# Kernel optimization log

Hardware: AMD Instinct MI355X
Metric: run time of the kernel (lower is better)

Reference implementation:

```python
import jax, jax.numpy as jnp
import numpy as np

B, K, N, D, H, NNEG, NTOP = 8, 8, 128, 256, 128, 64, 64
UNARY_SCALES = (1.0, 1.0, 1.0)  # one scale per tree level, tree_height = log2(K) = 3


def setup_inputs():
    key = jax.random.key(0)
    ks = jax.random.split(key, 8)
    s = 0.05
    return {
        'pos_fea': jax.random.normal(ks[0], (B, K, N, D), jnp.float32),
        'neg_fea': jax.random.normal(ks[1], (B * K, NNEG, D), jnp.float32),
        'pos_classes': jax.random.randint(ks[2], (B, K, N), 0, 20),
        'target_class': jax.random.randint(ks[3], (B,), 0, 20),
        'Wp1': jax.random.normal(ks[4], (2 * D, H), jnp.float32) * s,
        'bp1': jnp.zeros((H,), jnp.float32),
        'Wp2': jax.random.normal(ks[5], (H, 1), jnp.float32) * s,
        'bp2': jnp.zeros((1,), jnp.float32),
        'Wu1': jax.random.normal(ks[6], (2 * D, H), jnp.float32) * s,
        'bu1': jnp.zeros((H,), jnp.float32),
        'Wu2': jax.random.normal(ks[7], (H, 1), jnp.float32) * s,
        'bu2': jnp.zeros((1,), jnp.float32),
    }


def _relation(f0, f1, W1, b1, W2, b2):
    # RelationModule: Dense(H, relu) -> Dense(1) applied to concat([f0_m, f1_n])
    # for every cross pair; concat-Dense is split into two GEMMs. -> [Bn, M0, M1]
    d = f0.shape[-1]
    h0 = jnp.einsum('bmd,dh->bmh', f0, W1[:d])
    h1 = jnp.einsum('bnd,dh->bnh', f1, W1[d:])
    h = jax.nn.relu(h0[:, :, None, :] + h1[:, None, :, :] + b1)
    return jnp.einsum('bmnh,h->bmn', h, W2[:, 0]) + b2[0]


def _bg(t, idx):
    # batched_gather along axis 1: t [Bn, P, ...], idx [Bn, T]
    ie = idx.reshape(idx.shape + (1,) * (t.ndim - 2))
    ie = jnp.broadcast_to(ie, idx.shape + t.shape[2:])
    return jnp.take_along_axis(t, ie, axis=1)


def _rep(fea, sub):
    # subproblem representative feature: fea [Bn,S,N,D], sub [Bn,M,S] -> [Bn,M,D]
    idx = jnp.swapaxes(sub, 1, 2)[..., None]              # [Bn,S,M,1]
    idx = jnp.broadcast_to(idx, idx.shape[:-1] + (fea.shape[-1],))
    return jnp.take_along_axis(fea, idx, axis=2).mean(axis=1)


def _tree(pos_fea, neg_fea, Wp1, bp1, Wp2, bp2, Wu1, bu1, Wu2, bu2):
    pos_flat = pos_fea.reshape(B * K, N, D)
    # UnaryModule: mean relation score of each positive proposal vs the negative bag
    ue = _relation(pos_flat, neg_fea, Wu1, bu1, Wu2, bu2).mean(-1)   # [B*K, N]
    sub = jnp.broadcast_to(jnp.arange(N, dtype=jnp.int32)[None, :, None], (B * K, N, 1))
    pe = jnp.zeros_like(ue)
    tree_height = int(np.log2(K))
    best = None
    for i in range(tree_height):
        S = 2 ** i                      # subproblem size per branch at this level
        Bn = sub.shape[0] // 2
        M = sub.shape[1]
        sub2 = sub.reshape(Bn, 2, M, S)  # [::2] / [1::2] split of adjacent rows
        sub0, sub1 = sub2[:, 0], sub2[:, 1]
        pe2 = pe.reshape(Bn, 2, M)
        ue2 = ue.reshape(Bn, 2, M)
        fea = pos_flat.reshape(Bn, 2, S, N, D)
        rep0 = _rep(fea[:, 0], sub0)
        rep1 = _rep(fea[:, 1], sub1)
        # PairwiseCrossSimilarity: scores for all cross pairs of candidates
        scores = _relation(rep0, rep1, Wp1, bp1, Wp2, bp2).reshape(Bn, M * M)
        p0 = jnp.repeat(jnp.arange(M), M)
        p1 = jnp.tile(jnp.arange(M), M)
        pe = pe2[:, 0][:, p0] + pe2[:, 1][:, p1] - scores
        ue = ue2[:, 0][:, p0] + ue2[:, 1][:, p1]
        total = pe + UNARY_SCALES[i] * ue
        sub = jnp.concatenate([sub0[:, p0], sub1[:, p1]], axis=-1)  # [Bn, M*M, 2S]
        topk = 1 if i == tree_height - 1 else min(M * M, NTOP)
        _, inds = jax.lax.top_k(-total, topk)
        sub = _bg(sub, inds)
        ue = jnp.take_along_axis(ue, inds, axis=1)
        pe = jnp.take_along_axis(pe, inds, axis=1)
        best = jnp.take_along_axis(total, inds, axis=1)
    return sub, best


def reference(pos_fea, neg_fea, pos_classes, target_class,
              Wp1, bp1, Wp2, bp2, Wu1, bu1, Wu2, bu2):
    sub, _ = _tree(pos_fea, neg_fea, Wp1, bp1, Wp2, bp2, Wu1, bu1, Wu2, bu2)
    is_target = (pos_classes == target_class[:, None, None]).astype(jnp.float32)
    return sub[:, 0], is_target  # selected proposal per image [B,K], [B,K,N]
```

## Files before the change

### kernel.cpp

```cpp
#include <hip/hip_runtime.h>
#include <stdint.h>

#define B_ 8
#define K_ 8
#define N_ 128
#define D_ 256
#define H_ 128
#define NNEG_ 64

typedef unsigned long long u64;

__device__ __forceinline__ u64 shfl_xor_u64(u64 v, int m) {
    int lo = __shfl_xor((int)(unsigned)v, m, 64);
    int hi = __shfl_xor((int)(unsigned)(v >> 32), m, 64);
    return ((u64)(unsigned)hi << 32) | (unsigned)lo;
}
__device__ __forceinline__ u64 bitonic_merge64(u64 m, int lane) {
#pragma unroll
    for (int j = 32; j > 0; j >>= 1) {
        u64 o = shfl_xor_u64(m, j);
        bool keepMin = ((lane & j) == 0);
        bool lt = m < o;
        m = (keepMin == lt) ? m : o;
    }
    return m;
}
__device__ __forceinline__ u64 merge2(u64 a, u64 b, int lane) {
    u64 br = shfl_xor_u64(b, 63);
    u64 m = a < br ? a : br;
    return bitonic_merge64(m, lane);
}
__device__ __forceinline__ unsigned sortable(float f) {
    unsigned u = __float_as_uint(f);
    return (u & 0x80000000u) ? ~u : (u | 0x80000000u);
}
__device__ __forceinline__ float unsortable(unsigned u) {
    return __uint_as_float((u & 0x80000000u) ? (u & 0x7FFFFFFFu) : ~u);
}
__device__ __forceinline__ void sort128_reg(u64& v0, u64& v1, int lane) {
#pragma unroll
    for (int k = 2; k <= 64; k <<= 1) {
        bool d0 = ((lane & k) == 0);
        bool d1 = (k == 64) ? false : d0;
#pragma unroll
        for (int j = k >> 1; j > 0; j >>= 1) {
            u64 o0 = shfl_xor_u64(v0, j);
            bool km0 = (((lane & j) == 0) == d0);
            v0 = (km0 == (v0 < o0)) ? v0 : o0;
            u64 o1 = shfl_xor_u64(v1, j);
            bool km1 = (((lane & j) == 0) == d1);
            v1 = (km1 == (v1 < o1)) ? v1 : o1;
        }
    }
    if (v0 > v1) { u64 tmp = v0; v0 = v1; v1 = tmp; }
#pragma unroll
    for (int j = 32; j > 0; j >>= 1) {
        bool km = ((lane & j) == 0);
        u64 o0 = shfl_xor_u64(v0, j);
        v0 = (km == (v0 < o0)) ? v0 : o0;
        u64 o1 = shfl_xor_u64(v1, j);
        v1 = (km == (v1 < o1)) ? v1 : o1;
    }
}

__global__ __launch_bounds__(256) void g1_gemm(
    const float* __restrict__ pos, const float* __restrict__ neg,
    const float* __restrict__ Wu1, const float* __restrict__ Wp1,
    const int* __restrict__ pos_classes, const int* __restrict__ target_class,
    float* __restrict__ HU0, float* __restrict__ HU1n,
    float* __restrict__ HP0, float* __restrict__ HP1,
    float* __restrict__ outp) {
    int bid = blockIdx.x;
    int t = threadIdx.x;
    if (bid >= 896) {
        int base = (bid - 896) * 2048 + t * 8;
#pragma unroll
        for (int q = 0; q < 8; ++q) {
            int idx = base + q;
            outp[64 + idx] = (pos_classes[idx] == target_class[idx >> 10]) ? 1.0f : 0.0f;
        }
        return;
    }
    const float* A; const float* W; float* OUT; int bid2;
    if (bid < 256)      { A = pos; W = Wu1;           OUT = HU0;  bid2 = bid; }
    else if (bid < 384) { A = neg; W = Wu1 + D_ * H_; OUT = HU1n; bid2 = bid - 256; }
    else if (bid < 640) { A = pos; W = Wp1;           OUT = HP0;  bid2 = bid - 384; }
    else                { A = pos; W = Wp1 + D_ * H_; OUT = HP1;  bid2 = bid - 640; }
    int rb = (bid2 >> 1) * 64;
    int cb64 = (bid2 & 1) * 64;

    __shared__ float AsT[32][68];
    __shared__ float Bs[32][64];
    int tx = t & 15, ty = t >> 4;
    float acc[4][4];
#pragma unroll
    for (int i = 0; i < 4; ++i)
#pragma unroll
        for (int j = 0; j < 4; ++j) acc[i][j] = 0.f;

    for (int k0 = 0; k0 < D_; k0 += 32) {
#pragma unroll
        for (int rep = 0; rep < 2; ++rep) {
            int flat = t + rep * 256;
            int row = flat >> 3, kq = flat & 7;
            const float4 av = *(const float4*)&A[(size_t)(rb + row) * D_ + k0 + kq * 4];
            AsT[kq * 4 + 0][row] = av.x;
            AsT[kq * 4 + 1][row] = av.y;
            AsT[kq * 4 + 2][row] = av.z;
            AsT[kq * 4 + 3][row] = av.w;
        }
#pragma unroll
        for (int rep = 0; rep < 2; ++rep) {
            int flat = t + rep * 256;
            int kr = flat >> 4, cq = flat & 15;
            *(float4*)&Bs[kr][cq * 4] =
                *(const float4*)&W[(size_t)(k0 + kr) * H_ + cb64 + cq * 4];
        }
        __syncthreads();
#pragma unroll 8
        for (int kk = 0; kk < 32; ++kk) {
            const float4 av = *(const float4*)&AsT[kk][ty * 4];
            const float4 bv = *(const float4*)&Bs[kk][tx * 4];
            acc[0][0] += av.x * bv.x; acc[0][1] += av.x * bv.y;
            acc[0][2] += av.x * bv.z; acc[0][3] += av.x * bv.w;
            acc[1][0] += av.y * bv.x; acc[1][1] += av.y * bv.y;
            acc[1][2] += av.y * bv.z; acc[1][3] += av.y * bv.w;
            acc[2][0] += av.z * bv.x; acc[2][1] += av.z * bv.y;
            acc[2][2] += av.z * bv.z; acc[2][3] += av.z * bv.w;
            acc[3][0] += av.w * bv.x; acc[3][1] += av.w * bv.y;
            acc[3][2] += av.w * bv.z; acc[3][3] += av.w * bv.w;
        }
        __syncthreads();
    }
#pragma unroll
    for (int i = 0; i < 4; ++i) {
        float4 o = {acc[i][0], acc[i][1], acc[i][2], acc[i][3]};
        *(float4*)&OUT[(size_t)(rb + ty * 4 + i) * H_ + cb64 + tx * 4] = o;
    }
}

__global__ __launch_bounds__(256) void g2_ue_sc0(
    const float* __restrict__ HU0, const float* __restrict__ HU1n,
    const float* __restrict__ bu1, const float* __restrict__ Wu2,
    const float* __restrict__ bu2v,
    const float* __restrict__ HP0, const float* __restrict__ HP1,
    const float* __restrict__ bp1, const float* __restrict__ Wp2,
    const float* __restrict__ bp2,
    float* __restrict__ t0, float* __restrict__ sc0) {
    __shared__ float LsT[128][36];
    __shared__ float RsT[128][66];
    __shared__ float wsv[128];
    __shared__ float red[32][33];

    int bid = blockIdx.x;
    int t = threadIdx.x;
    bool is_ue = bid < 256;

    const float* Lsrc; const float* Rsrc; const float* b1v; const float* W2;
    if (is_ue) {
        int bk = bid >> 2, mt = bid & 3;
        Lsrc = HU0 + (size_t)(bk * N_ + mt * 32) * H_;
        Rsrc = HU1n + (size_t)bk * NNEG_ * H_;
        b1v = bu1; W2 = Wu2;
    } else {
        int bid2 = bid - 256;
        int b = bid2 >> 3, m0t = (bid2 >> 1) & 3, m1t = bid2 & 1;
        Lsrc = HP0 + (size_t)b * 2 * N_ * H_ + m0t * 32 * H_;
        Rsrc = HP1 + (size_t)b * 2 * N_ * H_ + N_ * H_ + m1t * 64 * H_;
        b1v = bp1; W2 = Wp2;
    }
    for (int i = t; i < 32 * 32; i += 256) {
        int m = i & 31, hq = i >> 5;
        const float4 a = *(const float4*)&Lsrc[(size_t)m * H_ + hq * 4];
        const float4 b = *(const float4*)&b1v[hq * 4];
        LsT[hq * 4 + 0][m] = a.x + b.x;
        LsT[hq * 4 + 1][m] = a.y + b.y;
        LsT[hq * 4 + 2][m] = a.z + b.z;
        LsT[hq * 4 + 3][m] = a.w + b.w;
    }
    for (int i = t; i < 64 * 32; i += 256) {
        int n = i & 63, hq = i >> 6;
        const float4 a = *(const float4*)&Rsrc[(size_t)n * H_ + hq * 4];
        RsT[hq * 4 + 0][n] = a.x;
        RsT[hq * 4 + 1][n] = a.y;
        RsT[hq * 4 + 2][n] = a.z;
        RsT[hq * 4 + 3][n] = a.w;
    }
    if (t < 128) wsv[t] = W2[t];
    __syncthreads();

    int tm = t & 7, tn = t >> 3;
    float a00 = 0.f, a01 = 0.f, a10 = 0.f, a11 = 0.f;
    float a20 = 0.f, a21 = 0.f, a30 = 0.f, a31 = 0.f;
#pragma unroll 4
    for (int h = 0; h < 128; ++h) {
        const float4 lv = *(const float4*)&LsT[h][tm * 4];
        const float2 rv = *(const float2*)&RsT[h][tn * 2];
        float w = wsv[h];
        float v;
        v = lv.x + rv.x; v = v > 0.f ? v : 0.f; a00 += v * w;
        v = lv.x + rv.y; v = v > 0.f ? v : 0.f; a01 += v * w;
        v = lv.y + rv.x; v = v > 0.f ? v : 0.f; a10 += v * w;
        v = lv.y + rv.y; v = v > 0.f ? v : 0.f; a11 += v * w;
        v = lv.z + rv.x; v = v > 0.f ? v : 0.f; a20 += v * w;
        v = lv.z + rv.y; v = v > 0.f ? v : 0.f; a21 += v * w;
        v = lv.w + rv.x; v = v > 0.f ? v : 0.f; a30 += v * w;
        v = lv.w + rv.y; v = v > 0.f ? v : 0.f; a31 += v * w;
    }

    if (is_ue) {
        int bk = bid >> 2, mt = bid & 3;
        red[tm * 4 + 0][tn] = a00 + a01;
        red[tm * 4 + 1][tn] = a10 + a11;
        red[tm * 4 + 2][tn] = a20 + a21;
        red[tm * 4 + 3][tn] = a30 + a31;
        __syncthreads();
        if (t < 32) {
            float s = 0.f;
            for (int q = 0; q < 32; ++q) s += red[t][q];
            t0[bk * N_ + mt * 32 + t] = s * (1.0f / NNEG_) + bu2v[0];
        }
    } else {
        int bid2 = bid - 256;
        int b = bid2 >> 3, m0t = (bid2 >> 1) & 3, m1t = bid2 & 1;
        float bp2v = bp2[0];
        float* orow = sc0 + (size_t)b * 16384;
        float accs[4][2] = {{a00, a01}, {a10, a11}, {a20, a21}, {a30, a31}};
#pragma unroll
        for (int i = 0; i < 4; ++i) {
            int m0 = m0t * 32 + tm * 4 + i;
#pragma unroll
            for (int j = 0; j < 2; ++j) {
                int m1 = m1t * 64 + tn * 2 + j;
                orow[m0 * 128 + m1] = accs[i][j] + bp2v;
            }
        }
    }
}

__global__ __launch_bounds__(256) void g3a_top0(const float* __restrict__ sc0,
                                                const float* __restrict__ t0,
                                                u64* __restrict__ g3c) {
    int bid = blockIdx.x;
    int r = bid >> 3, c = bid & 7;
    int t = threadIdx.x, lane = t & 63, w = t >> 6;
    __shared__ float tt[256];
    __shared__ u64 cand[4][128];
    if (t < 256) tt[t] = t0[r * 256 + t];
    __syncthreads();
    const float* row = sc0 + (size_t)r * 16384 + c * 2048 + w * 512;
    unsigned sv[8];
#pragma unroll
    for (int j = 0; j < 8; ++j) {
        int li = j * 64 + lane;
        int idx = c * 2048 + w * 512 + li;
        float v = (tt[idx >> 7] + tt[128 + (idx & 127)]) - row[li];
        sv[j] = sortable(v);
    }
    unsigned T = 0u;
#pragma unroll
    for (int it = 0; it < 16; ++it) {
        int p = 30 - 2 * it;
        unsigned C1 = T | (1u << p), C2 = T | (2u << p), C3 = T | (3u << p);
        unsigned c1 = 0u, c2 = 0u, c3 = 0u;
#pragma unroll
        for (int j = 0; j < 8; ++j) {
            c1 += (unsigned)__popcll(__ballot(sv[j] < C1));
            c2 += (unsigned)__popcll(__ballot(sv[j] < C2));
            c3 += (unsigned)__popcll(__ballot(sv[j] < C3));
        }
        unsigned k = (c3 < 64u) ? 3u : (c2 < 64u) ? 2u : (c1 < 64u) ? 1u : 0u;
        T |= (k << p);
    }
    u64* my = cand[w];
    int base = 0;
#pragma unroll
    for (int j = 0; j < 8; ++j) {
        u64 mask = __ballot(sv[j] <= T);
        if (sv[j] <= T) {
            int pos = base + (int)__popcll(mask & ((1ull << lane) - 1ull));
            if (pos < 128) {
                int idx = c * 2048 + w * 512 + j * 64 + lane;
                my[pos] = ((u64)sv[j] << 32) | (unsigned)idx;
            }
        }
        base += (int)__popcll(mask);
    }
    int cc = base < 128 ? base : 128;
    u64 v0 = (lane < cc) ? my[lane] : ~0ull;
    u64 v1 = (64 + lane < cc) ? my[64 + lane] : ~0ull;
    sort128_reg(v0, v1, lane);
    my[lane] = v0;
    __syncthreads();
    if (w == 0) {
        u64 x0 = cand[0][lane], x1 = cand[1][lane];
        u64 x2 = cand[2][lane], x3 = cand[3][lane];
        u64 y0 = merge2(x0, x1, lane), y1 = merge2(x2, x3, lane);
        g3c[(size_t)bid * 64 + lane] = merge2(y0, y1, lane);
    }
}

__global__ __launch_bounds__(256) void g4a_s1(
    const float* __restrict__ HP0, const float* __restrict__ HP1,
    const u64* __restrict__ g3c, int* __restrict__ pA,
    const float* __restrict__ bp1, const float* __restrict__ Wp2,
    const float* __restrict__ bp2, u64* __restrict__ g4top) {
    int bid = blockIdx.x;
    int u = bid >> 3, mq = (bid >> 1) & 3, nh = bid & 1;
    int t = threadIdx.x, lane = t & 63, w = t >> 6;
    __shared__ float LsT[128][17];
    __shared__ float RsT[128][34];
    __shared__ float taL[64], taR[64];
    __shared__ int paL[64], paR[64];
    __shared__ float wsv[128];
    __shared__ u64 cand[4][64];
    if (w < 2) {
        const u64* Lp = g3c + (size_t)(2 * u + w) * 512;
        u64 x0 = Lp[lane], x1 = Lp[64 + lane], x2 = Lp[128 + lane], x3 = Lp[192 + lane];
        u64 x4 = Lp[256 + lane], x5 = Lp[320 + lane], x6 = Lp[384 + lane], x7 = Lp[448 + lane];
        u64 y0 = merge2(x0, x1, lane), y1 = merge2(x2, x3, lane);
        u64 y2 = merge2(x4, x5, lane), y3 = merge2(x6, x7, lane);
        u64 z0 = merge2(y0, y1, lane), z1 = merge2(y2, y3, lane);
        u64 f = merge2(z0, z1, lane);
        int idx = (int)(f & 0xFFFFFFFFull);
        int pk = ((idx >> 7) << 8) | (idx & 127);
        float tv = unsortable((unsigned)(f >> 32));
        if (w == 0) { taL[lane] = tv; paL[lane] = pk; }
        else        { taR[lane] = tv; paR[lane] = pk; }
    }
    if (t >= 128) wsv[t - 128] = Wp2[t - 128];
    float bp2v = bp2[0];
    __syncthreads();
    if ((bid & 7) == 0) {
        if (t < 64) pA[(2 * u) * 64 + t] = paL[t];
        else if (t < 128) pA[(2 * u + 1) * 64 + (t - 64)] = paR[t - 64];
    }
    for (int i = t; i < 16 * 128; i += 256) {
        int m = i >> 7, h = i & 127;
        int pk = paL[mq * 16 + m]; int a0 = pk >> 8, a1 = pk & 255;
        float s = HP0[(size_t)(4 * u) * 16384 + a0 * 128 + h]
                + HP0[(size_t)(4 * u + 1) * 16384 + a1 * 128 + h];
        LsT[h][m] = s * 0.5f + bp1[h];
    }
    for (int i = t; i < 32 * 128; i += 256) {
        int n = i >> 7, h = i & 127;
        int pk = paR[nh * 32 + n]; int c0 = pk >> 8, c1 = pk & 255;
        float s = HP1[(size_t)(4 * u + 2) * 16384 + c0 * 128 + h]
                + HP1[(size_t)(4 * u + 3) * 16384 + c1 * 128 + h];
        RsT[h][n] = s * 0.5f;
    }
    __syncthreads();
    int lm = w * 4 + (lane >> 4);
    int ln = lane & 15;
    float a0 = 0.f, a1 = 0.f;
#pragma unroll 4
    for (int h = 0; h < 128; ++h) {
        float lv = LsT[h][lm];
        const float2 rv = *(const float2*)&RsT[h][ln * 2];
        float wv = wsv[h];
        float v;
        v = lv + rv.x; v = v > 0.f ? v : 0.f; a0 += v * wv;
        v = lv + rv.y; v = v > 0.f ? v : 0.f; a1 += v * wv;
    }
    int m_unit = mq * 16 + lm;
    int n0 = nh * 32 + ln * 2;
    float val0 = (taL[mq * 16 + lm] + taR[nh * 32 + ln * 2 + 0]) - (a0 + bp2v);
    float val1 = (taL[mq * 16 + lm] + taR[nh * 32 + ln * 2 + 1]) - (a1 + bp2v);
    u64 v0 = ((u64)sortable(val0) << 32) | (unsigned)(m_unit * 64 + n0);
    u64 v1 = ((u64)sortable(val1) << 32) | (unsigned)(m_unit * 64 + n0 + 1);
    sort128_reg(v0, v1, lane);
    cand[w][lane] = v0;
    __syncthreads();
    if (w == 0) {
        u64 x0 = cand[0][lane], x1 = cand[1][lane];
        u64 x2 = cand[2][lane], x3 = cand[3][lane];
        u64 y0 = merge2(x0, x1, lane), y1 = merge2(x2, x3, lane);
        g4top[(size_t)bid * 64 + lane] = merge2(y0, y1, lane);
    }
}

__global__ __launch_bounds__(256) void g4b_s2(
    const float* __restrict__ HP0, const float* __restrict__ HP1,
    const int* __restrict__ pA, const u64* __restrict__ g4top,
    const float* __restrict__ bp1, const float* __restrict__ Wp2,
    const float* __restrict__ bp2, float* __restrict__ outp) {
    int b = blockIdx.x;
    int t = threadIdx.x, lane = t & 63, w = t >> 6;
    __shared__ float LsT[128][68];
    __shared__ float RsT[128][36];
    __shared__ float tL[64], tR[64];
    __shared__ unsigned subL[64], subR[64];
    __shared__ float wsv[128];
    __shared__ u64 sred[4];
    if (t < 128) wsv[t] = Wp2[t];
    float bp2v = bp2[0];
    if (w < 2) {
        const u64* Lp = g4top + (size_t)(2 * b + w) * 512;
        u64 x0 = Lp[lane], x1 = Lp[64 + lane], x2 = Lp[128 + lane], x3 = Lp[192 + lane];
        u64 x4 = Lp[256 + lane], x5 = Lp[320 + lane], x6 = Lp[384 + lane], x7 = Lp[448 + lane];
        u64 y0 = merge2(x0, x1, lane), y1 = merge2(x2, x3, lane);
        u64 y2 = merge2(x4, x5, lane), y3 = merge2(x6, x7, lane);
        u64 z0 = merge2(y0, y1, lane), z1 = merge2(y2, y3, lane);
        u64 m = merge2(z0, z1, lane);
        int idx = (int)(m & 0xFFFFFFFFull);
        int p0 = idx >> 6, p1 = idx & 63;
        float val = unsortable((unsigned)(m >> 32));
        int rowL = 4 * b + 2 * w;
        int pkL = pA[rowL * 64 + p0];
        int pkR = pA[(rowL + 1) * 64 + p1];
        unsigned leaves = ((unsigned)pkL << 16) | (unsigned)pkR;
        if (w == 0) { tL[lane] = val; subL[lane] = leaves; }
        else        { tR[lane] = val; subR[lane] = leaves; }
    }
    __syncthreads();
    for (int i = t; i < 64 * 128; i += 256) {
        int m = i >> 7, h = i & 127;
        unsigned s4 = subL[m];
        float s = HP0[(size_t)(8 * b + 0) * 16384 + ((s4 >> 24) & 255u) * 128 + h]
                + HP0[(size_t)(8 * b + 1) * 16384 + ((s4 >> 16) & 255u) * 128 + h]
                + HP0[(size_t)(8 * b + 2) * 16384 + ((s4 >> 8) & 255u) * 128 + h]
                + HP0[(size_t)(8 * b + 3) * 16384 + (s4 & 255u) * 128 + h];
        LsT[h][m] = s * 0.25f + bp1[h];
    }
    u64 best = ~0ull;
    int qm = w * 4 + (lane >> 4);
    int qn = lane & 15;
    for (int half = 0; half < 2; ++half) {
        __syncthreads();
        for (int i = t; i < 32 * 128; i += 256) {
            int n = i >> 7, h = i & 127;
            int ng = half * 32 + n;
            unsigned s4 = subR[ng];
            float s = HP1[(size_t)(8 * b + 4) * 16384 + ((s4 >> 24) & 255u) * 128 + h]
                    + HP1[(size_t)(8 * b + 5) * 16384 + ((s4 >> 16) & 255u) * 128 + h]
                    + HP1[(size_t)(8 * b + 6) * 16384 + ((s4 >> 8) & 255u) * 128 + h]
                    + HP1[(size_t)(8 * b + 7) * 16384 + (s4 & 255u) * 128 + h];
            RsT[h][n] = s * 0.25f;
        }
        __syncthreads();
        float acc[4][2];
#pragma unroll
        for (int i = 0; i < 4; ++i) { acc[i][0] = 0.f; acc[i][1] = 0.f; }
#pragma unroll 2
        for (int h = 0; h < 128; ++h) {
            const float4 lv = *(const float4*)&LsT[h][qm * 4];
            const float2 rv = *(const float2*)&RsT[h][qn * 2];
            float wv = wsv[h];
            float v;
            v = lv.x + rv.x; v = v > 0.f ? v : 0.f; acc[0][0] += v * wv;
            v = lv.x + rv.y; v = v > 0.f ? v : 0.f; acc[0][1] += v * wv;
            v = lv.y + rv.x; v = v > 0.f ? v : 0.f; acc[1][0] += v * wv;
            v = lv.y + rv.y; v = v > 0.f ? v : 0.f; acc[1][1] += v * wv;
            v = lv.z + rv.x; v = v > 0.f ? v : 0.f; acc[2][0] += v * wv;
            v = lv.z + rv.y; v = v > 0.f ? v : 0.f; acc[2][1] += v * wv;
            v = lv.w + rv.x; v = v > 0.f ? v : 0.f; acc[3][0] += v * wv;
            v = lv.w + rv.y; v = v > 0.f ? v : 0.f; acc[3][1] += v * wv;
        }
#pragma unroll
        for (int mi = 0; mi < 4; ++mi) {
#pragma unroll
            for (int nj = 0; nj < 2; ++nj) {
                int m = qm * 4 + mi;
                int ng = half * 32 + qn * 2 + nj;
                float val = (tL[m] + tR[ng]) - (acc[mi][nj] + bp2v);
                u64 kk = ((u64)sortable(val) << 32) | (unsigned)(m * 64 + ng);
                best = kk < best ? kk : best;
            }
        }
    }
#pragma unroll
    for (int off = 32; off > 0; off >>= 1) {
        u64 o = shfl_xor_u64(best, off);
        best = o < best ? o : best;
    }
    if (lane == 0) sred[w] = best;
    __syncthreads();
    if (t == 0) {
        u64 bb = sred[0];
        for (int p = 1; p < 4; ++p) { u64 o = sred[p]; bb = o < bb ? o : bb; }
        int idx = (int)(bb & 0xFFFFFFFFull);
        unsigned sl = subL[idx >> 6], sr = subR[idx & 63];
        outp[b * 8 + 0] = (float)((sl >> 24) & 255u);
        outp[b * 8 + 1] = (float)((sl >> 16) & 255u);
        outp[b * 8 + 2] = (float)((sl >> 8) & 255u);
        outp[b * 8 + 3] = (float)(sl & 255u);
        outp[b * 8 + 4] = (float)((sr >> 24) & 255u);
        outp[b * 8 + 5] = (float)((sr >> 16) & 255u);
        outp[b * 8 + 6] = (float)((sr >> 8) & 255u);
        outp[b * 8 + 7] = (float)(sr & 255u);
    }
}

extern "C" void kernel_launch(void* const* d_in, const int* in_sizes, int n_in,
                              void* d_out, int out_size, void* d_ws, size_t ws_size,
                              hipStream_t stream) {
    const float* pos = (const float*)d_in[0];
    const float* neg = (const float*)d_in[1];
    const int* pos_classes = (const int*)d_in[2];
    const int* target_class = (const int*)d_in[3];
    const float* Wp1 = (const float*)d_in[4];
    const float* bp1 = (const float*)d_in[5];
    const float* Wp2 = (const float*)d_in[6];
    const float* bp2 = (const float*)d_in[7];
    const float* Wu1 = (const float*)d_in[8];
    const float* bu1 = (const float*)d_in[9];
    const float* Wu2 = (const float*)d_in[10];
    const float* bu2 = (const float*)d_in[11];

    float* wsf = (float*)d_ws;
    float* HU0 = wsf;
    float* HP0 = HU0 + 1048576;
    float* HP1 = HP0 + 1048576;
    float* HU1n = HP1 + 1048576;
    float* t0 = HU1n + 524288;
    float* sc0 = t0 + 8192;
    int* pA = (int*)(sc0 + 524288);
    u64* g3c = (u64*)wsf;
    u64* g4top = (u64*)wsf + 16384;
    float* outp = (float*)d_out;

    g1_gemm<<<900, 256, 0, stream>>>(pos, neg, Wu1, Wp1, pos_classes,
                                     target_class, HU0, HU1n, HP0, HP1, outp);
    g2_ue_sc0<<<512, 256, 0, stream>>>(HU0, HU1n, bu1, Wu2, bu2,
                                       HP0, HP1, bp1, Wp2, bp2, t0, sc0);
    g3a_top0<<<256, 256, 0, stream>>>(sc0, t0, g3c);
    g4a_s1<<<128, 256, 0, stream>>>(HP0, HP1, g3c, pA, bp1, Wp2, bp2, g4top);
    g4b_s2<<<8, 256, 0, stream>>>(HP0, HP1, pA, g4top, bp1, Wp2, bp2, outp);
}
```

Measured before the change: 174.4 us.

## Double-buffer g1 GEMM shared tiles and raise per-thread register tile to 4x8

The first GEMM kernel now uses 128 threads per block, each computing a 4x8 output tile instead of 4x4. Shared-memory A/B tiles are double-buffered, so the next K-chunk's global loads are issued into registers before the current chunk's FMA loop and stored to the alternate buffer afterward. This halves the barriers per chunk and hides global load latency. The cost is more registers and twice the shared memory per block, which could reduce occupancy. The tail blocks that write the is_target mask now handle 16 elements per thread to match the smaller block size.

```diff
diff --git a/kernel.cpp b/kernel.cpp
--- a/kernel.cpp
+++ b/kernel.cpp
@@ -63,7 +63,7 @@
     }
 }
 
-__global__ __launch_bounds__(256) void g1_gemm(
+__global__ __launch_bounds__(128) void g1_gemm(
     const float* __restrict__ pos, const float* __restrict__ neg,
     const float* __restrict__ Wu1, const float* __restrict__ Wp1,
     const int* __restrict__ pos_classes, const int* __restrict__ target_class,
@@ -73,9 +73,9 @@
     int bid = blockIdx.x;
     int t = threadIdx.x;
     if (bid >= 896) {
-        int base = (bid - 896) * 2048 + t * 8;
-#pragma unroll
-        for (int q = 0; q < 8; ++q) {
+        int base = (bid - 896) * 2048 + t * 16;
+#pragma unroll
+        for (int q = 0; q < 16; ++q) {
             int idx = base + q;
             outp[64 + idx] = (pos_classes[idx] == target_class[idx >> 10]) ? 1.0f : 0.0f;
         }
@@ -89,53 +89,92 @@
     int rb = (bid2 >> 1) * 64;
     int cb64 = (bid2 & 1) * 64;
 
-    __shared__ float AsT[32][68];
-    __shared__ float Bs[32][64];
-    int tx = t & 15, ty = t >> 4;
-    float acc[4][4];
+    __shared__ float AsT[2][32][68];
+    __shared__ float Bs[2][32][64];
+    int tx = t & 7, ty = t >> 3;
+    float acc[4][8];
 #pragma unroll
     for (int i = 0; i < 4; ++i)
 #pragma unroll
-        for (int j = 0; j < 4; ++j) acc[i][j] = 0.f;
-
-    for (int k0 = 0; k0 < D_; k0 += 32) {
-#pragma unroll
-        for (int rep = 0; rep < 2; ++rep) {
-            int flat = t + rep * 256;
-            int row = flat >> 3, kq = flat & 7;
-            const float4 av = *(const float4*)&A[(size_t)(rb + row) * D_ + k0 + kq * 4];
-            AsT[kq * 4 + 0][row] = av.x;
-            AsT[kq * 4 + 1][row] = av.y;
-            AsT[kq * 4 + 2][row] = av.z;
-            AsT[kq * 4 + 3][row] = av.w;
-        }
-#pragma unroll
-        for (int rep = 0; rep < 2; ++rep) {
-            int flat = t + rep * 256;
-            int kr = flat >> 4, cq = flat & 15;
-            *(float4*)&Bs[kr][cq * 4] =
-                *(const float4*)&W[(size_t)(k0 + kr) * H_ + cb64 + cq * 4];
-        }
-        __syncthreads();
+        for (int j = 0; j < 8; ++j) acc[i][j] = 0.f;
+
+#pragma unroll
+    for (int rep = 0; rep < 4; ++rep) {
+        int flat = t + rep * 128;
+        int row = flat >> 3, kq = flat & 7;
+        const float4 av = *(const float4*)&A[(size_t)(rb + row) * D_ + kq * 4];
+        AsT[0][kq * 4 + 0][row] = av.x;
+        AsT[0][kq * 4 + 1][row] = av.y;
+        AsT[0][kq * 4 + 2][row] = av.z;
+        AsT[0][kq * 4 + 3][row] = av.w;
+    }
+#pragma unroll
+    for (int rep = 0; rep < 4; ++rep) {
+        int flat = t + rep * 128;
+        int kr = flat >> 4, cq = flat & 15;
+        *(float4*)&Bs[0][kr][cq * 4] =
+            *(const float4*)&W[(size_t)kr * H_ + cb64 + cq * 4];
+    }
+    __syncthreads();
+
+    for (int chunk = 0; chunk < 8; ++chunk) {
+        int cur = chunk & 1, nxt = cur ^ 1;
+        bool pre = (chunk < 7);
+        int k0n = (chunk + 1) * 32;
+        float4 pa[4], pb[4];
+        if (pre) {
+#pragma unroll
+            for (int rep = 0; rep < 4; ++rep) {
+                int flat = t + rep * 128;
+                int row = flat >> 3, kq = flat & 7;
+                pa[rep] = *(const float4*)&A[(size_t)(rb + row) * D_ + k0n + kq * 4];
+            }
+#pragma unroll
+            for (int rep = 0; rep < 4; ++rep) {
+                int flat = t + rep * 128;
+                int kr = flat >> 4, cq = flat & 15;
+                pb[rep] = *(const float4*)&W[(size_t)(k0n + kr) * H_ + cb64 + cq * 4];
+            }
+        }
 #pragma unroll 8
         for (int kk = 0; kk < 32; ++kk) {
-            const float4 av = *(const float4*)&AsT[kk][ty * 4];
-            const float4 bv = *(const float4*)&Bs[kk][tx * 4];
-            acc[0][0] += av.x * bv.x; acc[0][1] += av.x * bv.y;
-            acc[0][2] += av.x * bv.z; acc[0][3] += av.x * bv.w;
-            acc[1][0] += av.y * bv.x; acc[1][1] += av.y * bv.y;
-            acc[1][2] += av.y * bv.z; acc[1][3] += av.y * bv.w;
-            acc[2][0] += av.z * bv.x; acc[2][1] += av.z * bv.y;
-            acc[2][2] += av.z * bv.z; acc[2][3] += av.z * bv.w;
-            acc[3][0] += av.w * bv.x; acc[3][1] += av.w * bv.y;
-            acc[3][2] += av.w * bv.z; acc[3][3] += av.w * bv.w;
+            const float4 av = *(const float4*)&AsT[cur][kk][ty * 4];
+            float bv[8];
+            *(float4*)&bv[0] = *(const float4*)&Bs[cur][kk][tx * 8];
+            *(float4*)&bv[4] = *(const float4*)&Bs[cur][kk][tx * 8 + 4];
+#pragma unroll
+            for (int j = 0; j < 8; ++j) {
+                acc[0][j] += av.x * bv[j];
+                acc[1][j] += av.y * bv[j];
+                acc[2][j] += av.z * bv[j];
+                acc[3][j] += av.w * bv[j];
+            }
+        }
+        if (pre) {
+#pragma unroll
+            for (int rep = 0; rep < 4; ++rep) {
+                int flat = t + rep * 128;
+                int row = flat >> 3, kq = flat & 7;
+                AsT[nxt][kq * 4 + 0][row] = pa[rep].x;
+                AsT[nxt][kq * 4 + 1][row] = pa[rep].y;
+                AsT[nxt][kq * 4 + 2][row] = pa[rep].z;
+                AsT[nxt][kq * 4 + 3][row] = pa[rep].w;
+            }
+#pragma unroll
+            for (int rep = 0; rep < 4; ++rep) {
+                int flat = t + rep * 128;
+                int kr = flat >> 4, cq = flat & 15;
+                *(float4*)&Bs[nxt][kr][cq * 4] = pb[rep];
+            }
         }
         __syncthreads();
     }
 #pragma unroll
     for (int i = 0; i < 4; ++i) {
-        float4 o = {acc[i][0], acc[i][1], acc[i][2], acc[i][3]};
-        *(float4*)&OUT[(size_t)(rb + ty * 4 + i) * H_ + cb64 + tx * 4] = o;
+        float4 o0 = {acc[i][0], acc[i][1], acc[i][2], acc[i][3]};
+        float4 o1 = {acc[i][4], acc[i][5], acc[i][6], acc[i][7]};
+        *(float4*)&OUT[(size_t)(rb + ty * 4 + i) * H_ + cb64 + tx * 8] = o0;
+        *(float4*)&OUT[(size_t)(rb + ty * 4 + i) * H_ + cb64 + tx * 8 + 4] = o1;
     }
 }
 
@@ -519,7 +558,7 @@
     u64* g4top = (u64*)wsf + 16384;
     float* outp = (float*)d_out;
 
-    g1_gemm<<<900, 256, 0, stream>>>(pos, neg, Wu1, Wp1, pos_classes,
+    g1_gemm<<<900, 128, 0, stream>>>(pos, neg, Wu1, Wp1, pos_classes,
                                      target_class, HU0, HU1n, HP0, HP1, outp);
     g2_ue_sc0<<<512, 256, 0, stream>>>(HU0, HU1n, bu1, Wu2, bu2,
                                        HP0, HP1, bp1, Wp2, bp2, t0, sc0);
```

Result: no change. 173.1 us (-0.7%).
